# Performance work log

Hardware: AMD Instinct MI355X
Metric: run time of the kernel (lower is better)

The kernel has to match this reference:

```python
import jax, jax.numpy as jnp
from jax import lax
import numpy as np

B, SQ, SK, H, NH, KS = 2, 2048, 2048, 1024, 16, 3
D = H // NH  # depth per head = 64


def setup_inputs() -> dict:
    key = jax.random.key(0)
    ks = jax.random.split(key, 10)
    s = 0.02
    return {
        "query_input": jax.random.normal(ks[0], (B, SQ, H), jnp.float32),
        "source_input": jax.random.normal(ks[1], (B, SK, H), jnp.float32),
        "mask": jnp.zeros((B, 1, 1, SK), jnp.float32),
        "Wq": jax.random.normal(ks[2], (KS, H, H), jnp.float32) * s,
        "bq": jnp.zeros((H,), jnp.float32),
        "Wk": jax.random.normal(ks[3], (KS, H, H), jnp.float32) * s,
        "bk": jnp.zeros((H,), jnp.float32),
        "Wv": jax.random.normal(ks[4], (KS, H, H), jnp.float32) * s,
        "bv": jnp.zeros((H,), jnp.float32),
        "Wo": jax.random.normal(ks[5], (H, H), jnp.float32) * s,
        "bo": jnp.zeros((H,), jnp.float32),
    }


def _conv1d_same(x, W, b):
    # x: [B, S, H], W: [KS, H_in, H_out] -> 'same' padded 1D conv
    y = lax.conv_general_dilated(x, W, window_strides=(1,), padding="SAME",
                                 dimension_numbers=("NWC", "WIO", "NWC"))
    return y + b


def _split_heads(x):
    # [B, S, H] -> [B, NH, S, D]
    b, s, _ = x.shape
    return x.reshape(b, s, NH, D).transpose(0, 2, 1, 3)


def reference(query_input, source_input, mask, Wq, bq, Wk, bk, Wv, bv, Wo, bo):
    q = _split_heads(_conv1d_same(query_input, Wq, bq)) * (D ** -0.5)
    k = _split_heads(_conv1d_same(source_input, Wk, bk))
    v = _split_heads(_conv1d_same(source_input, Wv, bv))
    logits = jnp.einsum("bhqd,bhkd->bhqk", q, k) + mask * (-1e9)
    weights = jax.nn.softmax(logits, axis=-1)  # dropout omitted (eval mode)
    attn = jnp.einsum("bhqk,bhkd->bhqd", weights, v)
    attn = attn.transpose(0, 2, 1, 3).reshape(q.shape[0], -1, H)
    return attn @ Wo + bo
```

## Files before the change

kernel.cpp:

```cpp
#include <hip/hip_runtime.h>
#include <stdint.h>

#define B_   2
#define S_   2048
#define H_   1024
#define NH_  16
#define D_   64
#define KC_  3072

typedef __attribute__((ext_vector_type(8))) short  short8;
typedef __attribute__((ext_vector_type(4))) float  floatx4;

typedef __attribute__((address_space(1))) const void gas_void;
typedef __attribute__((address_space(3))) void       las_void;

__device__ __forceinline__ void gld16(const void* g, void* l) {
    __builtin_amdgcn_global_load_lds((gas_void*)g, (las_void*)l, 16, 0, 0);
}

__device__ __forceinline__ unsigned short f2bf(float f) {
    union { float f; unsigned u; } v; v.f = f;
    unsigned r = v.u + 0x7fffu + ((v.u >> 16) & 1u);
    return (unsigned short)(r >> 16);
}

__global__ __launch_bounds__(256) void k_prep(
    const float* __restrict__ qin, const float* __restrict__ sin,
    const float* __restrict__ Wq, const float* __restrict__ Wk,
    const float* __restrict__ Wv, const float* __restrict__ Wo,
    unsigned short* __restrict__ xqp, unsigned short* __restrict__ xsp,
    unsigned short* __restrict__ Wqt, unsigned short* __restrict__ Wkt,
    unsigned short* __restrict__ Wvt, unsigned short* __restrict__ Wot) {
    int bid = blockIdx.x, tid = threadIdx.x;
    if (bid < 8200) {
        const float* src = (bid < 4100) ? qin : sin;
        unsigned short* dst = (bid < 4100) ? xqp : xsp;
        int b0 = (bid < 4100) ? bid : bid - 4100;
        int vid = (b0 * 256 + tid) * 4;
        if (vid >= B_ * 2050 * 1024) return;
        int row = vid >> 10;
        int b   = (row >= 2050) ? 1 : 0;
        int r   = row - b * 2050;
        int h   = vid & 1023;
        unsigned short o0 = 0, o1 = 0, o2 = 0, o3 = 0;
        if (r != 0 && r != 2049) {
            const float4 f = *(const float4*)(src + ((b * 2048 + r - 1) << 10) + h);
            o0 = f2bf(f.x); o1 = f2bf(f.y); o2 = f2bf(f.z); o3 = f2bf(f.w);
        }
        ushort4 o; o.x = o0; o.y = o1; o.z = o2; o.w = o3;
        *(ushort4*)(dst + vid) = o;
        return;
    }
    __shared__ float t[32][33];
    const float* src; unsigned short* dst; int R, bx, by;
    int tbid = bid - 8200;
    if (tbid < 9216) {
        int w = tbid / 3072, rem = tbid - w * 3072;
        src = (w == 0) ? Wq : (w == 1 ? Wk : Wv);
        dst = (w == 0) ? Wqt : (w == 1 ? Wkt : Wvt);
        R = 3072; bx = rem & 31; by = rem >> 5;
    } else {
        int rem = tbid - 9216;
        src = Wo; dst = Wot; R = 1024; bx = rem & 31; by = rem >> 5;
    }
    const int C = 1024;
    int c0 = bx * 32, r0 = by * 32;
    int tx = tid & 31, ty = tid >> 5;
#pragma unroll
    for (int k = 0; k < 4; ++k)
        t[ty + k * 8][tx] = src[(long)(r0 + ty + k * 8) * C + c0 + tx];
    __syncthreads();
#pragma unroll
    for (int k = 0; k < 4; ++k)
        dst[(long)(c0 + ty + k * 8) * R + r0 + tx] = f2bf(t[tx][ty + k * 8]);
}

__global__ __launch_bounds__(256) void k_conv_gemm(
    const unsigned short* __restrict__ xq, const unsigned short* __restrict__ xs,
    const unsigned short* __restrict__ Wqt, const unsigned short* __restrict__ Wkt,
    const unsigned short* __restrict__ Wvt,
    const float* __restrict__ bq, const float* __restrict__ bk, const float* __restrict__ bv,
    unsigned short* __restrict__ Qo, unsigned short* __restrict__ Ko,
    unsigned short* __restrict__ Vo) {
    int z = blockIdx.z;
    const unsigned short* X = (z == 0) ? xq : xs;
    const unsigned short* W = (z == 0) ? Wqt : (z == 1 ? Wkt : Wvt);
    const float* bias = (z == 0) ? bq : (z == 1 ? bk : bv);

    __shared__ unsigned short Al[520 * 8];
    __shared__ unsigned short Bl[1536 * 8];

    int n0 = blockIdx.x * 128, m0 = blockIdx.y * 128;
    int b = m0 >> 11;
    int tid = threadIdx.x, lane = tid & 63, w = tid >> 6;
    int quad = lane >> 4, l15 = lane & 15;
    int wm = w >> 1, wn = w & 1;

    floatx4 acc[4][4];
#pragma unroll
    for (int i = 0; i < 4; ++i)
#pragma unroll
        for (int j = 0; j < 4; ++j) acc[i][j] = (floatx4){0.f, 0.f, 0.f, 0.f};

    const unsigned short* Xbase = X + (m0 + 2 * b) * 1024;

    int aoff[3];
#pragma unroll
    for (int it = 0; it < 3; ++it) {
        int s = it * 256 + tid;
        if (s < 520) {
            int pr = s >> 3, p = s & 7, u = p ^ (pr & 7);
            aoff[it] = (pr * 2 + (u >> 2)) * 1024 + (u & 3) * 8;
        }
    }
    int boff[6];
#pragma unroll
    for (int it = 0; it < 6; ++it) {
        int s = it * 256 + tid;
        int tt = s >> 9, sp = s & 511;
        int pr = sp >> 3, p = sp & 7, u = p ^ (pr & 7);
        boff[it] = (n0 + pr * 2 + (u >> 2)) * KC_ + tt * 1024 + (u & 3) * 8;
    }

    for (int kt = 0; kt < 32; ++kt) {
        int k0 = kt * 32;
        gld16(Xbase + aoff[0] + k0, (char*)Al + tid * 16);
        gld16(Xbase + aoff[1] + k0, (char*)Al + (256 + tid) * 16);
        if (tid < 8)
            gld16(Xbase + aoff[2] + k0, (char*)Al + (512 + tid) * 16);
#pragma unroll
        for (int it = 0; it < 6; ++it)
            gld16(W + boff[it] + k0, (char*)Bl + (it * 256 + tid) * 16);
        __syncthreads();

#pragma unroll
        for (int t = 0; t < 3; ++t) {
            short8 af[4], bf[4];
#pragma unroll
            for (int i = 0; i < 4; ++i) {
                int r  = wm * 64 + i * 16 + l15 + t;
                int pr = r >> 1;
                int p  = (((r & 1) << 2) | quad) ^ (pr & 7);
                af[i]  = *(const short8*)(Al + (pr * 8 + p) * 8);
            }
#pragma unroll
            for (int j = 0; j < 4; ++j) {
                int n  = wn * 64 + j * 16 + l15;
                int pr = n >> 1;
                int p  = (((n & 1) << 2) | quad) ^ (pr & 7);
                bf[j]  = *(const short8*)(Bl + (t * 512 + pr * 8 + p) * 8);
            }
#pragma unroll
            for (int i = 0; i < 4; ++i)
#pragma unroll
                for (int j = 0; j < 4; ++j)
                    acc[i][j] = __builtin_amdgcn_mfma_f32_16x16x32_bf16(af[i], bf[j], acc[i][j], 0, 0, 0);
        }
        __syncthreads();
    }

#pragma unroll
    for (int j = 0; j < 4; ++j) {
        int n = n0 + wn * 64 + j * 16 + l15;
        float bb = bias[n];
        int nh = n >> 6, d = n & 63;
#pragma unroll
        for (int i = 0; i < 4; ++i) {
            int srow = (m0 & 2047) + wm * 64 + i * 16 + quad * 4;
#pragma unroll
            for (int r = 0; r < 4; ++r) {
                float v = acc[i][j][r] + bb;
                int s = srow + r;
                if (z == 0)
                    Qo[((b * NH_ + nh) * 2048 + s) * 64 + d] = f2bf(v * 0.125f);
                else if (z == 1)
                    Ko[((b * NH_ + nh) * 2048 + s) * 64 + d] = f2bf(v);
                else
                    Vo[((b * NH_ + nh) * 64 + d) * 2048 + s] = f2bf(v);
            }
        }
    }
}

__global__ __launch_bounds__(256) void k_flash(
    const unsigned short* __restrict__ Q, const unsigned short* __restrict__ K,
    const unsigned short* __restrict__ Vt, const float* __restrict__ mask,
    unsigned short* __restrict__ Ao) {
    __shared__ unsigned short Ul[128 * 136];
    __shared__ unsigned short Vl[64 * 128];

    int tid = threadIdx.x, w = tid >> 6, lane = tid & 63;
    int quad = lane >> 4, l15 = lane & 15;
    int bh = blockIdx.y;
    int b = bh >> 4, nh = bh & 15;
    int q0 = blockIdx.x * 128, wq = w * 32;

    short8 qf[2][2];
#pragma unroll
    for (int i = 0; i < 2; ++i)
#pragma unroll
        for (int kk = 0; kk < 2; ++kk)
            qf[i][kk] = *(const short8*)(Q + ((bh * 2048 + q0 + wq + i * 16 + l15) << 6) + kk * 32 + quad * 8);

    floatx4 oacc[2][4];
    float rsum[2][4];
#pragma unroll
    for (int i = 0; i < 2; ++i) {
#pragma unroll
        for (int j = 0; j < 4; ++j) oacc[i][j] = (floatx4){0.f, 0.f, 0.f, 0.f};
#pragma unroll
        for (int r = 0; r < 4; ++r) rsum[i][r] = 0.f;
    }
    const float* maskb = mask + b * S_;

    for (int kt = 0; kt < 16; ++kt) {
        int k0 = kt * 128;
#pragma unroll
        for (int it = 0; it < 4; ++it) {
            int e  = (it * 256 + tid) * 8;
            int kl = e >> 6;
            int c  = ((e >> 3) & 7) ^ (kl & 7);
            gld16(K + (bh * 2048 + k0 + kl) * 64 + c * 8, (char*)Ul + e * 2);
            int dl = e >> 7;
            int cp = (e >> 3) & 15;
            int c2 = (cp & 8) | ((cp ^ dl) & 7);
            gld16(Vt + (bh * 64 + dl) * 2048 + k0 + c2 * 8, (char*)Vl + e * 2);
        }
        __syncthreads();

        floatx4 sacc[2][8];
#pragma unroll
        for (int i = 0; i < 2; ++i)
#pragma unroll
            for (int j = 0; j < 8; ++j) sacc[i][j] = (floatx4){0.f, 0.f, 0.f, 0.f};
#pragma unroll
        for (int j = 0; j < 8; ++j) {
            int kl = j * 16 + l15;
            int cp0 = (0 * 4 + quad) ^ (kl & 7);
            short8 bf0 = *(const short8*)(Ul + kl * 64 + cp0 * 8);
            int cp1 = (1 * 4 + quad) ^ (kl & 7);
            short8 bf1 = *(const short8*)(Ul + kl * 64 + cp1 * 8);
#pragma unroll
            for (int i = 0; i < 2; ++i) {
                sacc[i][j] = __builtin_amdgcn_mfma_f32_16x16x32_bf16(qf[i][0], bf0, sacc[i][j], 0, 0, 0);
                sacc[i][j] = __builtin_amdgcn_mfma_f32_16x16x32_bf16(qf[i][1], bf1, sacc[i][j], 0, 0, 0);
            }
        }
        __syncthreads();

#pragma unroll
        for (int j = 0; j < 8; ++j) {
            float mv = maskb[k0 + j * 16 + l15] * (-1e9f);
#pragma unroll
            for (int i = 0; i < 2; ++i) {
                int row = wq + i * 16 + quad * 4;
#pragma unroll
                for (int r = 0; r < 4; ++r) {
                    float p = __expf(sacc[i][j][r] + mv);
                    rsum[i][r] += p;
                    Ul[(row + r) * 136 + j * 16 + l15] = f2bf(p);
                }
            }
        }

#pragma unroll
        for (int kk = 0; kk < 4; ++kk) {
            short8 af[2], bv4[4];
#pragma unroll
            for (int i = 0; i < 2; ++i)
                af[i] = *(const short8*)(Ul + (wq + i * 16 + l15) * 136 + kk * 32 + quad * 8);
#pragma unroll
            for (int j2 = 0; j2 < 4; ++j2) {
                int dl = j2 * 16 + l15;
                int c  = kk * 4 + quad;
                int cp = (c & 8) | ((c ^ dl) & 7);
                bv4[j2] = *(const short8*)(Vl + dl * 128 + cp * 8);
            }
#pragma unroll
            for (int i = 0; i < 2; ++i)
#pragma unroll
                for (int j2 = 0; j2 < 4; ++j2)
                    oacc[i][j2] = __builtin_amdgcn_mfma_f32_16x16x32_bf16(af[i], bv4[j2], oacc[i][j2], 0, 0, 0);
        }
        __syncthreads();
    }

#pragma unroll
    for (int i = 0; i < 2; ++i)
#pragma unroll
        for (int r = 0; r < 4; ++r) {
            float v = rsum[i][r];
            v += __shfl_xor(v, 1); v += __shfl_xor(v, 2);
            v += __shfl_xor(v, 4); v += __shfl_xor(v, 8);
            rsum[i][r] = 1.0f / v;
        }

#pragma unroll
    for (int i = 0; i < 2; ++i)
#pragma unroll
        for (int j2 = 0; j2 < 4; ++j2)
#pragma unroll
            for (int r = 0; r < 4; ++r) {
                int qrow = q0 + wq + i * 16 + quad * 4 + r;
                int hcol = nh * 64 + j2 * 16 + l15;
                Ao[(b * 2048 + qrow) * 1024 + hcol] = f2bf(oacc[i][j2][r] * rsum[i][r]);
            }
}

__global__ __launch_bounds__(256) void k_proj_gemm(
    const unsigned short* __restrict__ A, const unsigned short* __restrict__ Wt,
    const float* __restrict__ bo, float* __restrict__ out) {
    __shared__ unsigned short Al[2][64 * 64];
    __shared__ unsigned short Bl[2][128 * 64];

    int n0 = blockIdx.x * 128, m0 = blockIdx.y * 64;
    int tid = threadIdx.x, lane = tid & 63, w = tid >> 6;
    int quad = lane >> 4, l15 = lane & 15;
    int wm = w >> 1, wn = w & 1;

    floatx4 acc[2][4];
#pragma unroll
    for (int i = 0; i < 2; ++i)
#pragma unroll
        for (int j = 0; j < 4; ++j) acc[i][j] = (floatx4){0.f, 0.f, 0.f, 0.f};

    int ea[2], ao[2], eb[4], bof[4];
#pragma unroll
    for (int it = 0; it < 2; ++it) {
        int e  = (it * 256 + tid) * 8;
        int rl = e >> 6;
        int c  = ((e >> 3) & 7) ^ (rl & 7);
        ea[it] = e;
        ao[it] = (m0 + rl) * 1024 + c * 8;
    }
#pragma unroll
    for (int it = 0; it < 4; ++it) {
        int e  = (it * 256 + tid) * 8;
        int rl = e >> 6;
        int c  = ((e >> 3) & 7) ^ (rl & 7);
        eb[it] = e;
        bof[it] = (n0 + rl) * 1024 + c * 8;
    }

    auto stage = [&](int buf, int k0) {
#pragma unroll
        for (int it = 0; it < 2; ++it)
            gld16(A + ao[it] + k0, (char*)Al[buf] + ea[it] * 2);
#pragma unroll
        for (int it = 0; it < 4; ++it)
            gld16(Wt + bof[it] + k0, (char*)Bl[buf] + eb[it] * 2);
    };
    auto compute = [&](int buf) {
#pragma unroll
        for (int kk = 0; kk < 2; ++kk) {
            short8 af[2], bf[4];
#pragma unroll
            for (int i = 0; i < 2; ++i) {
                int m  = wm * 32 + i * 16 + l15;
                int cp = (kk * 4 + quad) ^ (m & 7);
                af[i]  = *(const short8*)(Al[buf] + m * 64 + cp * 8);
            }
#pragma unroll
            for (int j = 0; j < 4; ++j) {
                int n  = wn * 64 + j * 16 + l15;
                int cp = (kk * 4 + quad) ^ (n & 7);
                bf[j]  = *(const short8*)(Bl[buf] + n * 64 + cp * 8);
            }
#pragma unroll
            for (int i = 0; i < 2; ++i)
#pragma unroll
                for (int j = 0; j < 4; ++j)
                    acc[i][j] = __builtin_amdgcn_mfma_f32_16x16x32_bf16(af[i], bf[j], acc[i][j], 0, 0, 0);
        }
    };

    stage(0, 0);
    __syncthreads();
    for (int kt = 0; kt < 16; kt += 2) {
        if (kt + 1 < 16) stage(1, (kt + 1) * 64);
        compute(0);
        __syncthreads();
        if (kt + 2 < 16) stage(0, (kt + 2) * 64);
        compute(1);
        __syncthreads();
    }

#pragma unroll
    for (int j = 0; j < 4; ++j) {
        int n = n0 + wn * 64 + j * 16 + l15;
        float bb = bo[n];
#pragma unroll
        for (int i = 0; i < 2; ++i) {
            int m = m0 + wm * 32 + i * 16 + quad * 4;
#pragma unroll
            for (int r = 0; r < 4; ++r)
                out[(m + r) * 1024 + n] = acc[i][j][r] + bb;
        }
    }
}

extern "C" void kernel_launch(void* const* d_in, const int* in_sizes, int n_in,
                              void* d_out, int out_size, void* d_ws, size_t ws_size,
                              hipStream_t stream) {
    (void)in_sizes; (void)n_in; (void)out_size; (void)ws_size;
    const float* q_in = (const float*)d_in[0];
    const float* s_in = (const float*)d_in[1];
    const float* mask = (const float*)d_in[2];
    const float* Wq   = (const float*)d_in[3];
    const float* bq   = (const float*)d_in[4];
    const float* Wk   = (const float*)d_in[5];
    const float* bk   = (const float*)d_in[6];
    const float* Wv   = (const float*)d_in[7];
    const float* bv   = (const float*)d_in[8];
    const float* Wo   = (const float*)d_in[9];
    const float* bo   = (const float*)d_in[10];
    float* out = (float*)d_out;

    char* ws = (char*)d_ws;
    size_t off = 0;
    auto alloc = [&](size_t bytes) {
        char* p = ws + off;
        off += (bytes + 255) & ~(size_t)255;
        return p;
    };
    unsigned short* xqp = (unsigned short*)alloc((size_t)B_ * 2050 * 1024 * 2);
    unsigned short* xsp = (unsigned short*)alloc((size_t)B_ * 2050 * 1024 * 2);
    unsigned short* Wqt = (unsigned short*)alloc((size_t)KC_ * H_ * 2);
    unsigned short* Wkt = (unsigned short*)alloc((size_t)KC_ * H_ * 2);
    unsigned short* Wvt = (unsigned short*)alloc((size_t)KC_ * H_ * 2);
    unsigned short* Wot = (unsigned short*)alloc((size_t)H_ * H_ * 2);
    unsigned short* Qb  = (unsigned short*)alloc((size_t)B_ * NH_ * S_ * D_ * 2);
    unsigned short* Kb  = (unsigned short*)alloc((size_t)B_ * NH_ * S_ * D_ * 2);
    unsigned short* Vtb = (unsigned short*)alloc((size_t)B_ * NH_ * S_ * D_ * 2);
    unsigned short* Ab  = (unsigned short*)alloc((size_t)B_ * S_ * H_ * 2);

    k_prep<<<18440, 256, 0, stream>>>(q_in, s_in, Wq, Wk, Wv, Wo,
                                      xqp, xsp, Wqt, Wkt, Wvt, Wot);
    k_conv_gemm<<<dim3(8, 32, 3), 256, 0, stream>>>(xqp, xsp, Wqt, Wkt, Wvt,
                                                    bq, bk, bv, Qb, Kb, Vtb);
    k_flash<<<dim3(16, 32), 256, 0, stream>>>(Qb, Kb, Vtb, mask, Ab);
    k_proj_gemm<<<dim3(8, 64), 256, 0, stream>>>(Ab, Wot, bo, out);
}
```

Before: 325.4 us.

## Deepen conv GEMM K-tile and transpose attention MFMA operands for vectorized stores

The conv GEMM now loads a 64-wide K slice per iteration (16 iterations instead of 32) with a row-major XOR-swizzled LDS layout, halving barrier count per K at the cost of more LDS. The attention kernel swaps MFMA operand order so each lane holds a query row's consecutive keys, so probability writes, mask loads and output stores become 4-wide vector accesses. The row-sum reduction shrinks to two shuffles. An extra barrier was added between the P write and the PV read.

New measurement: 322.8 us. About the same (-0.8%).

```diff
diff --git a/kernel.cpp b/kernel.cpp
--- a/kernel.cpp
+++ b/kernel.cpp
@@ -87,8 +87,8 @@
     const unsigned short* W = (z == 0) ? Wqt : (z == 1 ? Wkt : Wvt);
     const float* bias = (z == 0) ? bq : (z == 1 ? bk : bv);
 
-    __shared__ unsigned short Al[520 * 8];
-    __shared__ unsigned short Bl[1536 * 8];
+    __shared__ unsigned short Al[132 * 64];
+    __shared__ unsigned short Bl[3 * 128 * 64];
 
     int n0 = blockIdx.x * 128, m0 = blockIdx.y * 128;
     int b = m0 >> 11;
@@ -104,57 +104,73 @@
 
     const unsigned short* Xbase = X + (m0 + 2 * b) * 1024;
 
-    int aoff[3];
-#pragma unroll
-    for (int it = 0; it < 3; ++it) {
-        int s = it * 256 + tid;
-        if (s < 520) {
-            int pr = s >> 3, p = s & 7, u = p ^ (pr & 7);
-            aoff[it] = (pr * 2 + (u >> 2)) * 1024 + (u & 3) * 8;
-        }
-    }
-    int boff[6];
-#pragma unroll
-    for (int it = 0; it < 6; ++it) {
-        int s = it * 256 + tid;
-        int tt = s >> 9, sp = s & 511;
-        int pr = sp >> 3, p = sp & 7, u = p ^ (pr & 7);
-        boff[it] = (n0 + pr * 2 + (u >> 2)) * KC_ + tt * 1024 + (u & 3) * 8;
-    }
-
-    for (int kt = 0; kt < 32; ++kt) {
-        int k0 = kt * 32;
-        gld16(Xbase + aoff[0] + k0, (char*)Al + tid * 16);
-        gld16(Xbase + aoff[1] + k0, (char*)Al + (256 + tid) * 16);
-        if (tid < 8)
-            gld16(Xbase + aoff[2] + k0, (char*)Al + (512 + tid) * 16);
-#pragma unroll
-        for (int it = 0; it < 6; ++it)
-            gld16(W + boff[it] + k0, (char*)Bl + (it * 256 + tid) * 16);
+    int eaA[4], oaA[4];
+#pragma unroll
+    for (int it = 0; it < 4; ++it) {
+        int e  = (it * 256 + tid) * 8;
+        int r  = e >> 6;
+        int cp = (e >> 3) & 7;
+        int c  = cp ^ (r & 7);
+        eaA[it] = e;
+        oaA[it] = r * 1024 + c * 8;
+    }
+    int eaX = 0, oaX = 0;
+    if (tid < 16) {
+        int e  = (1024 + tid) * 8;
+        int r  = 128 + (tid >> 3);
+        int cp = tid & 7;
+        int c  = cp ^ (r & 7);
+        eaX = e;
+        oaX = r * 1024 + c * 8;
+    }
+    int eaB[12], oaB[12];
+#pragma unroll
+    for (int it = 0; it < 12; ++it) {
+        int e  = (it * 256 + tid) * 8;
+        int t  = e >> 13;
+        int er = e & 8191;
+        int rl = er >> 6;
+        int cp = (er >> 3) & 7;
+        int c  = cp ^ (rl & 7);
+        eaB[it] = e;
+        oaB[it] = (n0 + rl) * KC_ + t * 1024 + c * 8;
+    }
+
+    for (int kt = 0; kt < 16; ++kt) {
+        int k0 = kt * 64;
+#pragma unroll
+        for (int it = 0; it < 4; ++it)
+            gld16(Xbase + oaA[it] + k0, (char*)Al + eaA[it] * 2);
+        if (tid < 16)
+            gld16(Xbase + oaX + k0, (char*)Al + eaX * 2);
+#pragma unroll
+        for (int it = 0; it < 12; ++it)
+            gld16(W + oaB[it] + k0, (char*)Bl + eaB[it] * 2);
         __syncthreads();
 
 #pragma unroll
         for (int t = 0; t < 3; ++t) {
-            short8 af[4], bf[4];
-#pragma unroll
-            for (int i = 0; i < 4; ++i) {
-                int r  = wm * 64 + i * 16 + l15 + t;
-                int pr = r >> 1;
-                int p  = (((r & 1) << 2) | quad) ^ (pr & 7);
-                af[i]  = *(const short8*)(Al + (pr * 8 + p) * 8);
-            }
-#pragma unroll
-            for (int j = 0; j < 4; ++j) {
-                int n  = wn * 64 + j * 16 + l15;
-                int pr = n >> 1;
-                int p  = (((n & 1) << 2) | quad) ^ (pr & 7);
-                bf[j]  = *(const short8*)(Bl + (t * 512 + pr * 8 + p) * 8);
-            }
-#pragma unroll
-            for (int i = 0; i < 4; ++i)
-#pragma unroll
-                for (int j = 0; j < 4; ++j)
-                    acc[i][j] = __builtin_amdgcn_mfma_f32_16x16x32_bf16(af[i], bf[j], acc[i][j], 0, 0, 0);
+#pragma unroll
+            for (int kk = 0; kk < 2; ++kk) {
+                short8 af[4], bf[4];
+#pragma unroll
+                for (int i = 0; i < 4; ++i) {
+                    int r  = wm * 64 + i * 16 + l15 + t;
+                    int cp = (kk * 4 + quad) ^ (r & 7);
+                    af[i]  = *(const short8*)(Al + r * 64 + cp * 8);
+                }
+#pragma unroll
+                for (int j = 0; j < 4; ++j) {
+                    int n  = wn * 64 + j * 16 + l15;
+                    int cp = (kk * 4 + quad) ^ (n & 7);
+                    bf[j]  = *(const short8*)(Bl + t * 8192 + n * 64 + cp * 8);
+                }
+#pragma unroll
+                for (int i = 0; i < 4; ++i)
+#pragma unroll
+                    for (int j = 0; j < 4; ++j)
+                        acc[i][j] = __builtin_amdgcn_mfma_f32_16x16x32_bf16(af[i], bf[j], acc[i][j], 0, 0, 0);
+            }
         }
         __syncthreads();
     }
@@ -203,14 +219,11 @@
             qf[i][kk] = *(const short8*)(Q + ((bh * 2048 + q0 + wq + i * 16 + l15) << 6) + kk * 32 + quad * 8);
 
     floatx4 oacc[2][4];
-    float rsum[2][4];
-#pragma unroll
-    for (int i = 0; i < 2; ++i) {
-#pragma unroll
-        for (int j = 0; j < 4; ++j) oacc[i][j] = (floatx4){0.f, 0.f, 0.f, 0.f};
-#pragma unroll
-        for (int r = 0; r < 4; ++r) rsum[i][r] = 0.f;
-    }
+    float rsum[2] = {0.f, 0.f};
+#pragma unroll
+    for (int i = 0; i < 2; ++i)
+#pragma unroll
+        for (int m = 0; m < 4; ++m) oacc[i][m] = (floatx4){0.f, 0.f, 0.f, 0.f};
     const float* maskb = mask + b * S_;
 
     for (int kt = 0; kt < 16; ++kt) {
@@ -232,79 +245,79 @@
 #pragma unroll
         for (int i = 0; i < 2; ++i)
 #pragma unroll
-            for (int j = 0; j < 8; ++j) sacc[i][j] = (floatx4){0.f, 0.f, 0.f, 0.f};
-#pragma unroll
-        for (int j = 0; j < 8; ++j) {
-            int kl = j * 16 + l15;
-            int cp0 = (0 * 4 + quad) ^ (kl & 7);
-            short8 bf0 = *(const short8*)(Ul + kl * 64 + cp0 * 8);
-            int cp1 = (1 * 4 + quad) ^ (kl & 7);
-            short8 bf1 = *(const short8*)(Ul + kl * 64 + cp1 * 8);
+            for (int jb = 0; jb < 8; ++jb) sacc[i][jb] = (floatx4){0.f, 0.f, 0.f, 0.f};
+#pragma unroll
+        for (int jb = 0; jb < 8; ++jb) {
+            int kl = jb * 16 + l15;
+            int cp0 = quad ^ (kl & 7);
+            short8 af0 = *(const short8*)(Ul + kl * 64 + cp0 * 8);
+            int cp1 = (4 + quad) ^ (kl & 7);
+            short8 af1 = *(const short8*)(Ul + kl * 64 + cp1 * 8);
 #pragma unroll
             for (int i = 0; i < 2; ++i) {
-                sacc[i][j] = __builtin_amdgcn_mfma_f32_16x16x32_bf16(qf[i][0], bf0, sacc[i][j], 0, 0, 0);
-                sacc[i][j] = __builtin_amdgcn_mfma_f32_16x16x32_bf16(qf[i][1], bf1, sacc[i][j], 0, 0, 0);
-            }
-        }
-        __syncthreads();
-
-#pragma unroll
-        for (int j = 0; j < 8; ++j) {
-            float mv = maskb[k0 + j * 16 + l15] * (-1e9f);
-#pragma unroll
-            for (int i = 0; i < 2; ++i) {
-                int row = wq + i * 16 + quad * 4;
-#pragma unroll
-                for (int r = 0; r < 4; ++r) {
-                    float p = __expf(sacc[i][j][r] + mv);
-                    rsum[i][r] += p;
-                    Ul[(row + r) * 136 + j * 16 + l15] = f2bf(p);
-                }
-            }
-        }
+                sacc[i][jb] = __builtin_amdgcn_mfma_f32_16x16x32_bf16(af0, qf[i][0], sacc[i][jb], 0, 0, 0);
+                sacc[i][jb] = __builtin_amdgcn_mfma_f32_16x16x32_bf16(af1, qf[i][1], sacc[i][jb], 0, 0, 0);
+            }
+        }
+        __syncthreads();
+
+#pragma unroll
+        for (int i = 0; i < 2; ++i) {
+            int qrow = wq + i * 16 + l15;
+#pragma unroll
+            for (int jb = 0; jb < 8; ++jb) {
+                const float4 mv4 = *(const float4*)(maskb + k0 + jb * 16 + quad * 4);
+                float p0 = __expf(sacc[i][jb][0] + mv4.x * (-1e9f));
+                float p1 = __expf(sacc[i][jb][1] + mv4.y * (-1e9f));
+                float p2 = __expf(sacc[i][jb][2] + mv4.z * (-1e9f));
+                float p3 = __expf(sacc[i][jb][3] + mv4.w * (-1e9f));
+                rsum[i] += (p0 + p1) + (p2 + p3);
+                ushort4 pk;
+                pk.x = f2bf(p0); pk.y = f2bf(p1); pk.z = f2bf(p2); pk.w = f2bf(p3);
+                *(ushort4*)(Ul + qrow * 136 + jb * 16 + quad * 4) = pk;
+            }
+        }
+        __syncthreads();
 
 #pragma unroll
         for (int kk = 0; kk < 4; ++kk) {
-            short8 af[2], bv4[4];
-#pragma unroll
-            for (int i = 0; i < 2; ++i)
-                af[i] = *(const short8*)(Ul + (wq + i * 16 + l15) * 136 + kk * 32 + quad * 8);
-#pragma unroll
-            for (int j2 = 0; j2 < 4; ++j2) {
-                int dl = j2 * 16 + l15;
+            short8 av[4], bp[2];
+#pragma unroll
+            for (int m = 0; m < 4; ++m) {
+                int dl = m * 16 + l15;
                 int c  = kk * 4 + quad;
                 int cp = (c & 8) | ((c ^ dl) & 7);
-                bv4[j2] = *(const short8*)(Vl + dl * 128 + cp * 8);
+                av[m]  = *(const short8*)(Vl + dl * 128 + cp * 8);
             }
 #pragma unroll
             for (int i = 0; i < 2; ++i)
-#pragma unroll
-                for (int j2 = 0; j2 < 4; ++j2)
-                    oacc[i][j2] = __builtin_amdgcn_mfma_f32_16x16x32_bf16(af[i], bv4[j2], oacc[i][j2], 0, 0, 0);
-        }
-        __syncthreads();
-    }
-
-#pragma unroll
-    for (int i = 0; i < 2; ++i)
-#pragma unroll
-        for (int r = 0; r < 4; ++r) {
-            float v = rsum[i][r];
-            v += __shfl_xor(v, 1); v += __shfl_xor(v, 2);
-            v += __shfl_xor(v, 4); v += __shfl_xor(v, 8);
-            rsum[i][r] = 1.0f / v;
-        }
-
-#pragma unroll
-    for (int i = 0; i < 2; ++i)
-#pragma unroll
-        for (int j2 = 0; j2 < 4; ++j2)
-#pragma unroll
-            for (int r = 0; r < 4; ++r) {
-                int qrow = q0 + wq + i * 16 + quad * 4 + r;
-                int hcol = nh * 64 + j2 * 16 + l15;
-                Ao[(b * 2048 + qrow) * 1024 + hcol] = f2bf(oacc[i][j2][r] * rsum[i][r]);
-            }
+                bp[i] = *(const short8*)(Ul + (wq + i * 16 + l15) * 136 + kk * 32 + quad * 8);
+#pragma unroll
+            for (int i = 0; i < 2; ++i)
+#pragma unroll
+                for (int m = 0; m < 4; ++m)
+                    oacc[i][m] = __builtin_amdgcn_mfma_f32_16x16x32_bf16(av[m], bp[i], oacc[i][m], 0, 0, 0);
+        }
+        __syncthreads();
+    }
+
+#pragma unroll
+    for (int i = 0; i < 2; ++i) {
+        float v = rsum[i];
+        v += __shfl_xor(v, 16);
+        v += __shfl_xor(v, 32);
+        float inv = 1.0f / v;
+        int qrow = q0 + wq + i * 16 + l15;
+#pragma unroll
+        for (int m = 0; m < 4; ++m) {
+            ushort4 o;
+            o.x = f2bf(oacc[i][m][0] * inv);
+            o.y = f2bf(oacc[i][m][1] * inv);
+            o.z = f2bf(oacc[i][m][2] * inv);
+            o.w = f2bf(oacc[i][m][3] * inv);
+            *(ushort4*)(Ao + (b * 2048 + qrow) * 1024 + nh * 64 + m * 16 + quad * 4) = o;
+        }
+    }
 }
 
 __global__ __launch_bounds__(256) void k_proj_gemm(
```
